# Optimization experiments

Measured on AMD Instinct MI355X. Metric: run time of the kernel, lower is better.

The kernel has to match this reference:

```python
import jax, jax.numpy as jnp
import numpy as np

DIM = 1024
HEADS = 16
DHEAD = 64
MAXLEN = 512
B = 8
N = 256   # sequence (x) length
M = 256   # memory (h) length; M + N <= MAXLEN
INNER = HEADS * DHEAD


def setup_inputs() -> dict:
    key = jax.random.key(0)
    ks = jax.random.split(key, 8)
    w = lambda k, shape: jax.random.normal(k, shape, jnp.float32) * 0.02
    return {
        "x": jax.random.normal(ks[0], (B, N, DIM), jnp.float32),
        "h": jax.random.normal(ks[1], (B, M, DIM), jnp.float32),
        "Wqkv": w(ks[2], (DIM, 3 * INNER)),
        "Wkr": w(ks[3], (DIM, INNER)),
        "R": jax.random.normal(ks[4], (2 * MAXLEN, DIM), jnp.float32),
        "u": jax.random.normal(ks[5], (DHEAD,), jnp.float32),
        "v": jax.random.normal(ks[6], (DHEAD,), jnp.float32),
        "Wout": w(ks[7], (INNER, DIM)),
        "max_len": MAXLEN,
    }


def reference(x, h, Wqkv, Wkr, R, u, v, Wout, max_len):
    b, n, dim = x.shape
    m = h.shape[1]
    t = m + n
    scale = DHEAD ** -0.5

    cat = jnp.concatenate([h, x], axis=1)                     # [b, t, dim]
    qkv = cat @ Wqkv                                          # [b, t, 3*inner]
    q, k, val = [s.reshape(b, t, HEADS, DHEAD).transpose(0, 2, 1, 3)
                 for s in jnp.split(qkv, 3, axis=-1)]          # [b, h, t, d]

    # shifts[i, j] = (j - i) mod 2L, sliced as in the torch buffer
    ar = jnp.arange(2 * max_len)
    shifts_full = (ar[None, :] - ar[:, None]) % (2 * max_len)
    shifts = shifts_full[:max_len, :max_len][m:m + n, :t]      # [n, t]

    kr = (R @ Wkr)[shifts]                                    # gather: [n, t, inner]
    kr = kr.reshape(n, t, HEADS, DHEAD).transpose(2, 0, 1, 3)  # [h, n, t, d]

    q = q[:, :, m:]                                           # [b, h, n, d]

    term_a = jnp.einsum('bhnd,bhmd->bhnm', q, k)
    term_b = jnp.einsum('bhnd,hnmd->bhnm', q, kr)
    term_c = jnp.einsum('d,bhmd->bhm', u, k)[:, :, None, :]    # broadcast over n
    term_d = jnp.einsum('d,hnmd->hnm', v, kr)[None]            # broadcast over b
    dots = (term_a + term_b + term_c + term_d) * scale         # [b, h, n, t]

    qi = jnp.arange(n)[:, None]
    jm = jnp.arange(m)[None, :]
    js = jnp.arange(n)[None, :]
    mem_mask = jnp.where(qi > jm, -jnp.inf, 0.0)               # [n, m]
    ar_mask = jnp.where(js > qi, -jnp.inf, 0.0)                # [n, n]
    bias = jnp.concatenate([mem_mask, ar_mask], axis=1)[None, None]  # [1,1,n,t]

    attn = jax.nn.softmax(dots + bias, axis=-1)
    out = jnp.einsum('bhnm,bhmd->bhnd', attn, val)             # [b, h, n, d]
    out = out.transpose(0, 2, 1, 3).reshape(b, n, INNER)
    return out @ Wout
```

## Files before the change

kernel.cpp:

```cpp
#include <hip/hip_runtime.h>
#include <hip/hip_bf16.h>
#include <math.h>

typedef unsigned short u16;
typedef short bf16x8 __attribute__((ext_vector_type(8)));
typedef float f32x4 __attribute__((ext_vector_type(4)));

__device__ __forceinline__ u16 f2b(float f) {
    __hip_bfloat16 h = __float2bfloat16(f);
    return *reinterpret_cast<u16*>(&h);
}
__device__ __forceinline__ float b2f(u16 v) {
    __hip_bfloat16 h;
    *reinterpret_cast<u16*>(&h) = v;
    return __bfloat162float(h);
}

__device__ __forceinline__ void gload_lds16(const void* g, void* l) {
    __builtin_amdgcn_global_load_lds(
        (const __attribute__((address_space(1))) void*)g,
        (__attribute__((address_space(3))) void*)l, 16, 0, 0);
}


struct EpiQKV4 {
    u16 *Q, *Kt, *Vt;
    __device__ void operator()(int rowp, int colp, f32x4 vals) const {
        int b = colp >> 9, pos = colp & 511;
        int sec = rowp >> 10, cc = rowp & 1023;
        int head = cc >> 6, d0 = cc & 63;
        if (sec == 0) {
            if (pos < 256) return;
            ushort4 o;
            o.x = f2b(vals[0] * 0.125f); o.y = f2b(vals[1] * 0.125f);
            o.z = f2b(vals[2] * 0.125f); o.w = f2b(vals[3] * 0.125f);
            *(ushort4*)(Q + (long)((head * 8 + b) * 256 + (pos - 256)) * 64 + d0) = o;
        } else if (sec == 1) {
            ushort4 o;
            o.x = f2b(vals[0]); o.y = f2b(vals[1]);
            o.z = f2b(vals[2]); o.w = f2b(vals[3]);
            *(ushort4*)(Kt + (long)((b * 16 + head) * 512 + pos) * 64 + d0) = o;
        } else {
            #pragma unroll
            for (int r = 0; r < 4; ++r)
                Vt[(long)((b * 16 + head) * 64 + d0 + r) * 512 + pos] = f2b(vals[r]);
        }
    }
};

struct EpiStoreBf {
    u16* C; long ldc; long strideZ;
    __device__ void operator()(int z, int row, int col, float val) const {
        C[(long)z * strideZ + (long)row * ldc + col] = f2b(val);
    }
};


template <typename Epi, bool AF32, bool ROWMAP>
__device__ __forceinline__ void gemm_bt_body(char* smem, int bx, int by, int bz,
                                             const void* __restrict__ Av, int lda, long strideAz,
                                             const u16* __restrict__ B, int ldb, long strideBz,
                                             int K, Epi epi) {
    constexpr int LDT = 56;
    u16* As = (u16*)smem;
    u16* Bs = As + 64 * LDT;
    int n0 = bx * 64, m0 = by * 64, z = bz;
    const u16* Bb = B + (long)z * strideBz + (long)n0 * ldb;
    int tid = threadIdx.x;
    int wave = tid >> 6, lane = tid & 63;
    int wm = wave >> 1, wn = wave & 1;
    int lrow = lane & 15, lquad = lane >> 4;
    int srow = tid >> 2, scol = (tid & 3) * 8;
    f32x4 acc[2][2] = {};
    for (int k0 = 0; k0 < K; k0 += 32) {
        if constexpr (AF32) {
            long arow = m0 + srow;
            if constexpr (ROWMAP) arow = (arow < 256) ? 768 + arow : 0;
            const float* src = (const float*)Av + (long)z * strideAz + arow * lda + k0 + scol;
            float4 f0 = *(const float4*)src;
            float4 f1 = *(const float4*)(src + 4);
            bf16x8 vv;
            vv[0] = (short)f2b(f0.x); vv[1] = (short)f2b(f0.y);
            vv[2] = (short)f2b(f0.z); vv[3] = (short)f2b(f0.w);
            vv[4] = (short)f2b(f1.x); vv[5] = (short)f2b(f1.y);
            vv[6] = (short)f2b(f1.z); vv[7] = (short)f2b(f1.w);
            *(bf16x8*)(As + srow * LDT + scol) = vv;
        } else {
            const u16* Ab = (const u16*)Av + (long)z * strideAz + (long)m0 * lda;
            *(bf16x8*)(As + srow * LDT + scol) = *(const bf16x8*)(Ab + (long)srow * lda + k0 + scol);
        }
        *(bf16x8*)(Bs + srow * LDT + scol) = *(const bf16x8*)(Bb + (long)srow * ldb + k0 + scol);
        __syncthreads();
        bf16x8 af[2], bfr[2];
        #pragma unroll
        for (int mt = 0; mt < 2; ++mt)
            af[mt] = *(const bf16x8*)(As + (wm * 32 + mt * 16 + lrow) * LDT + lquad * 8);
        #pragma unroll
        for (int nt = 0; nt < 2; ++nt)
            bfr[nt] = *(const bf16x8*)(Bs + (wn * 32 + nt * 16 + lrow) * LDT + lquad * 8);
        #pragma unroll
        for (int mt = 0; mt < 2; ++mt)
            #pragma unroll
            for (int nt = 0; nt < 2; ++nt)
                acc[mt][nt] = __builtin_amdgcn_mfma_f32_16x16x32_bf16(af[mt], bfr[nt], acc[mt][nt], 0, 0, 0);
        __syncthreads();
    }
    #pragma unroll
    for (int mt = 0; mt < 2; ++mt)
        #pragma unroll
        for (int nt = 0; nt < 2; ++nt)
            #pragma unroll
            for (int r = 0; r < 4; ++r) {
                int row = m0 + wm * 32 + mt * 16 + lquad * 4 + r;
                int col = n0 + wn * 32 + nt * 16 + lrow;
                epi(z, row, col, acc[mt][nt][r]);
            }
}

__global__ __launch_bounds__(256) void prep_kernel(const float* __restrict__ x,
                                                   const float* __restrict__ h,
                                                   u16* __restrict__ catBF,
                                                   const float* __restrict__ Wqkv, u16* __restrict__ WqkvT,
                                                   const float* __restrict__ Wkr,  u16* __restrict__ WkrT,
                                                   const float* __restrict__ Wout, u16* __restrict__ WoutT,
                                                   u16* __restrict__ vtGuard) {
    __shared__ float tile[32][33];
    int bid = blockIdx.x, tid = threadIdx.x;
    if (bid == 7168) {
        ((unsigned int*)vtGuard)[tid] = 0u;
        return;
    }
    if (bid < 2048) {
        int idx = (bid * 256 + tid) * 8;
        int c = idx & 1023, r = idx >> 10;
        int b = r >> 9, pos = r & 511;
        const float* src = (pos < 256) ? h + ((long)(b * 256 + pos) * 1024 + c)
                                       : x + ((long)(b * 256 + pos - 256) * 1024 + c);
        float4 f0 = *(const float4*)src;
        float4 f1 = *(const float4*)(src + 4);
        bf16x8 vv;
        vv[0] = (short)f2b(f0.x); vv[1] = (short)f2b(f0.y);
        vv[2] = (short)f2b(f0.z); vv[3] = (short)f2b(f0.w);
        vv[4] = (short)f2b(f1.x); vv[5] = (short)f2b(f1.y);
        vv[6] = (short)f2b(f1.z); vv[7] = (short)f2b(f1.w);
        *(bf16x8*)(catBF + idx) = vv;
        return;
    }
    const float* W; u16* WT; int nb, kb;
    if (bid < 5120) {
        int w = bid - 2048;
        W = Wqkv; WT = WqkvT;
        nb = (w % 96) * 32; kb = (w / 96) * 32;
        int tx = tid & 31, ty = tid >> 5;
        #pragma unroll
        for (int i = 0; i < 32; i += 8)
            tile[ty + i][tx] = W[(long)(kb + ty + i) * 3072 + nb + tx];
    } else {
        int w = bid - 5120;
        if (w < 1024) { W = Wkr; WT = WkrT; }
        else          { W = Wout; WT = WoutT; w -= 1024; }
        nb = (w & 31) * 32; kb = (w >> 5) * 32;
        int tx = tid & 31, ty = tid >> 5;
        #pragma unroll
        for (int i = 0; i < 32; i += 8)
            tile[ty + i][tx] = W[(long)(kb + ty + i) * 1024 + nb + tx];
    }
    __syncthreads();
    int row = tid >> 3;
    int c4 = (tid & 7) * 4;
    ushort4 o;
    o.x = f2b(tile[c4 + 0][row]);
    o.y = f2b(tile[c4 + 1][row]);
    o.z = f2b(tile[c4 + 2][row]);
    o.w = f2b(tile[c4 + 3][row]);
    *(ushort4*)(WT + (long)(nb + row) * 1024 + kb + c4) = o;
}

__global__ __launch_bounds__(256, 5) void qkv_rwg_kernel(const u16* __restrict__ A, const u16* __restrict__ B,
                                                         EpiQKV4 eq,
                                                         const float* __restrict__ R, const u16* __restrict__ WkrT,
                                                         u16* __restrict__ RWg) {
    __shared__ alignas(16) char smem[24576];
    int bid0 = blockIdx.x;
    if (bid0 < 80) {
        gemm_bt_body<EpiStoreBf, true, true>(smem, bid0 & 15, bid0 >> 4, 0,
            (const void*)R, 1024, 0L, WkrT, 1024, 0L, 1024, EpiStoreBf{RWg, 1024, 0});
        return;
    }
    int q = bid0 - 80;
    int xcd = q & 7, s = q >> 3;
    int G = xcd * 10 + (s >> 4);
    int w = s & 15;
    int m0, n0;
    if (G < 64) {
        int nchunk = G >> 4, mrow = G & 15;
        m0 = 1024 + mrow * 128 + (w & 1) * 64;
        n0 = (nchunk * 8 + (w >> 1)) * 128;
    } else {
        int G2 = G - 64;
        int nchunk = G2 >> 3, mrow = G2 & 7;
        m0 = mrow * 128 + (w & 1) * 64;
        int c = nchunk * 8 + (w >> 1);
        n0 = (c >> 1) * 512 + 256 + (c & 1) * 128;
    }
    int tid = threadIdx.x, wave = tid >> 6, lane = tid & 63;
    int lrow = lane & 15, lquad = lane >> 4;
    const u16* Ab = A + (long)m0 * 1024;
    const u16* Bb = B + (long)n0 * 1024;
    f32x4 acc[4][2] = {};

    auto stage = [&](int buf, int k0) {
        u16* Asb = (u16*)smem + buf * 6144;
        u16* Bsb = Asb + 2048;
        int row = tid >> 2, col = k0 + (tid & 3) * 8;
        gload_lds16(Ab + (long)row * 1024 + col, Asb + tid * 8);
        #pragma unroll
        for (int i = 0; i < 2; ++i)
            gload_lds16(Bb + (long)(i * 64 + row) * 1024 + col, Bsb + i * 2048 + tid * 8);
    };
    auto compute = [&](int buf) {
        u16* Asb = (u16*)smem + buf * 6144;
        u16* Bsb = Asb + 2048;
        bf16x8 af[4], bfr[2];
        #pragma unroll
        for (int mt = 0; mt < 4; ++mt)
            af[mt] = *(const bf16x8*)(Asb + (mt * 16 + lrow) * 32 + lquad * 8);
        #pragma unroll
        for (int nt = 0; nt < 2; ++nt)
            bfr[nt] = *(const bf16x8*)(Bsb + (wave * 32 + nt * 16 + lrow) * 32 + lquad * 8);
        #pragma unroll
        for (int mt = 0; mt < 4; ++mt)
            #pragma unroll
            for (int nt = 0; nt < 2; ++nt)
                acc[mt][nt] = __builtin_amdgcn_mfma_f32_16x16x32_bf16(af[mt], bfr[nt], acc[mt][nt], 0, 0, 0);
    };

    stage(0, 0);
    stage(1, 32);
    for (int t = 0; t < 31; ++t) {
        asm volatile("s_waitcnt vmcnt(3)" ::: "memory");
        __builtin_amdgcn_sched_barrier(0);
        __builtin_amdgcn_s_barrier();
        __builtin_amdgcn_sched_barrier(0);
        compute(t & 1);
        __builtin_amdgcn_sched_barrier(0);
        __builtin_amdgcn_s_barrier();
        __builtin_amdgcn_sched_barrier(0);
        if (t < 30) stage(t & 1, (t + 2) * 32);
    }
    asm volatile("s_waitcnt vmcnt(0)" ::: "memory");
    __builtin_amdgcn_sched_barrier(0);
    __builtin_amdgcn_s_barrier();
    __builtin_amdgcn_sched_barrier(0);
    compute(1);

    #pragma unroll
    for (int mt = 0; mt < 4; ++mt)
        #pragma unroll
        for (int nt = 0; nt < 2; ++nt) {
            int rowp = m0 + mt * 16 + lquad * 4;
            int colp = n0 + wave * 32 + nt * 16 + lrow;
            eq(rowp, colp, acc[mt][nt]);
        }
}

__global__ __launch_bounds__(256, 4) void outproj_kernel(const u16* __restrict__ A,
                                                         const u16* __restrict__ B,
                                                         float* __restrict__ out) {
    __shared__ alignas(16) char smem[16384];
    int bid = blockIdx.x;
    int n0 = (bid & 15) * 64, m0 = (bid >> 4) * 64;
    int tid = threadIdx.x, wave = tid >> 6, lane = tid & 63;
    int wm = wave >> 1, wn = wave & 1;
    int lrow = lane & 15, lquad = lane >> 4;
    const u16* Ab = A + (long)m0 * 1024;
    const u16* Bb = B + (long)n0 * 1024;
    f32x4 acc[2][2] = {};

    auto stage = [&](int buf, int k0) {
        u16* Asb = (u16*)smem + buf * 4096;
        u16* Bsb = Asb + 2048;
        int row = tid >> 2, col = k0 + (tid & 3) * 8;
        gload_lds16(Ab + (long)row * 1024 + col, Asb + tid * 8);
        gload_lds16(Bb + (long)row * 1024 + col, Bsb + tid * 8);
    };
    auto compute = [&](int buf) {
        u16* Asb = (u16*)smem + buf * 4096;
        u16* Bsb = Asb + 2048;
        bf16x8 af[2], bfr[2];
        #pragma unroll
        for (int mt = 0; mt < 2; ++mt)
            af[mt] = *(const bf16x8*)(Asb + (wm * 32 + mt * 16 + lrow) * 32 + lquad * 8);
        #pragma unroll
        for (int nt = 0; nt < 2; ++nt)
            bfr[nt] = *(const bf16x8*)(Bsb + (wn * 32 + nt * 16 + lrow) * 32 + lquad * 8);
        #pragma unroll
        for (int mt = 0; mt < 2; ++mt)
            #pragma unroll
            for (int nt = 0; nt < 2; ++nt)
                acc[mt][nt] = __builtin_amdgcn_mfma_f32_16x16x32_bf16(af[mt], bfr[nt], acc[mt][nt], 0, 0, 0);
    };

    stage(0, 0);
    stage(1, 32);
    for (int t = 0; t < 31; ++t) {
        asm volatile("s_waitcnt vmcnt(2)" ::: "memory");
        __builtin_amdgcn_sched_barrier(0);
        __builtin_amdgcn_s_barrier();
        __builtin_amdgcn_sched_barrier(0);
        compute(t & 1);
        __builtin_amdgcn_sched_barrier(0);
        __builtin_amdgcn_s_barrier();
        __builtin_amdgcn_sched_barrier(0);
        if (t < 30) stage(t & 1, (t + 2) * 32);
    }
    asm volatile("s_waitcnt vmcnt(0)" ::: "memory");
    __builtin_amdgcn_sched_barrier(0);
    __builtin_amdgcn_s_barrier();
    __builtin_amdgcn_sched_barrier(0);
    compute(1);

    #pragma unroll
    for (int mt = 0; mt < 2; ++mt)
        #pragma unroll
        for (int nt = 0; nt < 2; ++nt)
            #pragma unroll
            for (int r = 0; r < 4; ++r)
                out[(long)(m0 + wm * 32 + mt * 16 + lquad * 4 + r) * 1024
                    + n0 + wn * 32 + nt * 16 + lrow] = acc[mt][nt][r];
}

__global__ __launch_bounds__(256, 4) void attn_kernel(const u16* __restrict__ Qs,
                                                      const u16* __restrict__ Kt,
                                                      const u16* __restrict__ VT,
                                                      const u16* __restrict__ RWg,
                                                      const float* __restrict__ uvec,
                                                      const float* __restrict__ vvec,
                                                      u16* __restrict__ attnOut) {
    constexpr int LDSW = 328;
    __shared__ alignas(16) u16 SQ[32 * LDSW];
    __shared__ float red[2][4][32];
    int id = blockIdx.x;
    int bh = id & 127, it = id >> 7;
    int b = bh >> 4, h = bh & 15;
    int i0 = it * 32;
    int w0 = i0;
    int tid = threadIdx.x, wave = tid >> 6, lane = tid & 63;
    int lrow = lane & 15, lquad = lane >> 4;

    bf16x8 aq[2][2], aqv[2][2];
    #pragma unroll
    for (int iu = 0; iu < 2; ++iu) {
        const u16* qbase = Qs + (long)((h * 8 + b) * 256 + i0 + iu * 16 + lrow) * 64;
        bf16x8 q0 = *(const bf16x8*)(qbase + lquad * 8);
        bf16x8 q1 = *(const bf16x8*)(qbase + 32 + lquad * 8);
        #pragma unroll
        for (int j = 0; j < 8; ++j) {
            float f0 = b2f((u16)q0[j]), f1 = b2f((u16)q1[j]);
            aq[iu][0][j]  = (short)f2b(f0 + 0.125f * uvec[lquad * 8 + j]);
            aq[iu][1][j]  = (short)f2b(f1 + 0.125f * uvec[32 + lquad * 8 + j]);
            aqv[iu][0][j] = (short)f2b(f0 + 0.125f * vvec[lquad * 8 + j]);
            aqv[iu][1][j] = (short)f2b(f1 + 0.125f * vvec[32 + lquad * 8 + j]);
        }
    }

    const u16* rwbase = RWg + (long)(wave * 80) * 1024 + h * 64;
    #pragma unroll
    for (int t = 0; t < 5; ++t) {
        const u16* rp = rwbase + (long)(t * 16 + lrow) * 1024;
        bf16x8 br0 = *(const bf16x8*)(rp + lquad * 8);
        bf16x8 br1 = *(const bf16x8*)(rp + 32 + lquad * 8);
        int sc = wave * 80 + t * 16 + lrow;
        #pragma unroll
        for (int iu = 0; iu < 2; ++iu) {
            f32x4 qa = {0.f, 0.f, 0.f, 0.f};
            qa = __builtin_amdgcn_mfma_f32_16x16x32_bf16(aqv[iu][0], br0, qa, 0, 0, 0);
            qa = __builtin_amdgcn_mfma_f32_16x16x32_bf16(aqv[iu][1], br1, qa, 0, 0, 0);
            #pragma unroll
            for (int r = 0; r < 4; ++r)
                SQ[(iu * 16 + lquad * 4 + r) * LDSW + sc] = f2b(qa[r]);
        }
    }

    const u16* kbase = Kt + ((long)bh * 512 + w0 + wave * 80) * 64;
    bf16x8 bk0[5], bk1[5];
    #pragma unroll
    for (int t = 0; t < 5; ++t) {
        const u16* kp = kbase + (long)(t * 16 + lrow) * 64;
        bk0[t] = *(const bf16x8*)(kp + lquad * 8);
        bk1[t] = *(const bf16x8*)(kp + 32 + lquad * 8);
    }
    f32x4 acc[2][5];
    #pragma unroll
    for (int t = 0; t < 5; ++t)
        #pragma unroll
        for (int iu = 0; iu < 2; ++iu) {
            f32x4 a = {0.f, 0.f, 0.f, 0.f};
            a = __builtin_amdgcn_mfma_f32_16x16x32_bf16(aq[iu][0], bk0[t], a, 0, 0, 0);
            a = __builtin_amdgcn_mfma_f32_16x16x32_bf16(aq[iu][1], bk1[t], a, 0, 0, 0);
            acc[iu][t] = a;
        }
    __syncthreads();

    float m4[2][4];
    #pragma unroll
    for (int iu = 0; iu < 2; ++iu)
        #pragma unroll
        for (int r = 0; r < 4; ++r) m4[iu][r] = -1e30f;
    #pragma unroll
    for (int t = 0; t < 5; ++t) {
        int lj = wave * 80 + t * 16 + lrow;
        #pragma unroll
        for (int iu = 0; iu < 2; ++iu)
            #pragma unroll
            for (int r = 0; r < 4; ++r) {
                int rloc = iu * 16 + lquad * 4 + r;
                int d = lj - rloc;
                int dc = d < 0 ? 0 : (d > 256 ? 256 : d);
                bool ok = (unsigned)d <= 256u;
                float val = ok ? acc[iu][t][r] + b2f(SQ[rloc * LDSW + dc]) : -1e30f;
                acc[iu][t][r] = val;
                m4[iu][r] = fmaxf(m4[iu][r], val);
            }
    }
    #pragma unroll
    for (int iu = 0; iu < 2; ++iu)
        #pragma unroll
        for (int r = 0; r < 4; ++r) {
            #pragma unroll
            for (int off = 1; off < 16; off <<= 1)
                m4[iu][r] = fmaxf(m4[iu][r], __shfl_xor(m4[iu][r], off));
            if (lrow == 0) red[0][wave][iu * 16 + lquad * 4 + r] = m4[iu][r];
        }
    __syncthreads();

    float gmax[2][4];
    #pragma unroll
    for (int iu = 0; iu < 2; ++iu)
        #pragma unroll
        for (int r = 0; r < 4; ++r) {
            int row = iu * 16 + lquad * 4 + r;
            gmax[iu][r] = fmaxf(fmaxf(red[0][0][row], red[0][1][row]),
                                fmaxf(red[0][2][row], red[0][3][row]));
        }

    float s4[2][4] = {};
    #pragma unroll
    for (int t = 0; t < 5; ++t) {
        int lj = wave * 80 + t * 16 + lrow;
        #pragma unroll
        for (int iu = 0; iu < 2; ++iu)
            #pragma unroll
            for (int r = 0; r < 4; ++r) {
                float p = __expf(acc[iu][t][r] - gmax[iu][r]);
                s4[iu][r] += p;
                SQ[(iu * 16 + lquad * 4 + r) * LDSW + lj] = f2b(p);
            }
    }
    #pragma unroll
    for (int iu = 0; iu < 2; ++iu)
        #pragma unroll
        for (int r = 0; r < 4; ++r) {
            #pragma unroll
            for (int off = 1; off < 16; off <<= 1)
                s4[iu][r] += __shfl_xor(s4[iu][r], off);
            if (lrow == 0) red[1][wave][iu * 16 + lquad * 4 + r] = s4[iu][r];
        }
    __syncthreads();

    const u16* vbase = VT + ((long)bh * 64 + wave * 16 + lrow) * 512 + w0;
    f32x4 oacc[2] = {};
    bf16x8 vp[10];
    #pragma unroll
    for (int t = 0; t < 10; ++t)
        vp[t] = *(const bf16x8*)(vbase + t * 32 + lquad * 8);
    #pragma unroll
    for (int t = 0; t < 10; ++t)
        #pragma unroll
        for (int iu = 0; iu < 2; ++iu) {
            bf16x8 ap = *(const bf16x8*)(SQ + (iu * 16 + lrow) * LDSW + t * 32 + lquad * 8);
            oacc[iu] = __builtin_amdgcn_mfma_f32_16x16x32_bf16(ap, vp[t], oacc[iu], 0, 0, 0);
        }
    #pragma unroll
    for (int iu = 0; iu < 2; ++iu)
        #pragma unroll
        for (int r = 0; r < 4; ++r) {
            int row = iu * 16 + lquad * 4 + r;
            float inv = 1.0f / (red[1][0][row] + red[1][1][row] + red[1][2][row] + red[1][3][row]);
            attnOut[(long)(b * 256 + i0 + row) * 1024 + h * 64 + wave * 16 + lrow] = f2b(oacc[iu][r] * inv);
        }
}


extern "C" void kernel_launch(void* const* d_in, const int* in_sizes, int n_in,
                              void* d_out, int out_size, void* d_ws, size_t ws_size,
                              hipStream_t stream) {
    (void)in_sizes; (void)n_in; (void)out_size; (void)ws_size;
    const float* x    = (const float*)d_in[0];
    const float* h    = (const float*)d_in[1];
    const float* Wqkv = (const float*)d_in[2];
    const float* Wkr  = (const float*)d_in[3];
    const float* R    = (const float*)d_in[4];
    const float* u    = (const float*)d_in[5];
    const float* v    = (const float*)d_in[6];
    const float* Wout = (const float*)d_in[7];
    float* out = (float*)d_out;

    char* ws = (char*)d_ws;
    size_t off = 0;
    auto alloc = [&](size_t bytes) -> void* {
        void* p = ws + off;
        off = (off + bytes + 255) & ~(size_t)255;
        return p;
    };
    u16* catBF  = (u16*)alloc(4096L * 1024 * 2);
    u16* WqkvT  = (u16*)alloc(3072L * 1024 * 2);
    u16* WkrT   = (u16*)alloc(1024L * 1024 * 2);
    u16* WoutT  = (u16*)alloc(1024L * 1024 * 2);
    u16* RWg    = (u16*)alloc(320L * 1024 * 2);
    u16* Q      = (u16*)alloc(16L * 8 * 256 * 64 * 2);
    u16* Kt     = (u16*)alloc(8L * 16 * 512 * 64 * 2);
    u16* VT     = (u16*)alloc(8L * 16 * 64 * 512 * 2 + 1024);
    u16* attnO  = (u16*)alloc(2048L * 1024 * 2);
    u16* vtGuard = VT + 8L * 16 * 64 * 512;

    prep_kernel<<<7169, 256, 0, stream>>>(x, h, catBF, Wqkv, WqkvT, Wkr, WkrT, Wout, WoutT, vtGuard);
    qkv_rwg_kernel<<<1360, 256, 0, stream>>>(WqkvT, catBF, EpiQKV4{Q, Kt, VT}, R, WkrT, RWg);
    attn_kernel<<<1024, 256, 0, stream>>>(Q, Kt, VT, RWg, u, v, attnO);
    outproj_kernel<<<512, 256, 0, stream>>>(attnO, WoutT, out);
}
```

Measured before the change: 168.8 us.

## Enlarge QKV GEMM tiles to 128x128, swizzle LDS, set MFMA priority in attention

The QKV GEMM block tile grows from 64x128 to 128x128, with a 2x2 wave layout and 4x4 MFMA accumulators per wave. This halves the grid and raises operand reuse per LDS load. An XOR-like column permutation is applied when staging global-to-LDS in both the QKV and out-projection GEMMs, with matching reads, to reduce LDS bank conflicts. The RWg blocks move to the end of the grid, and s_setprio is raised around the MFMA loops in the attention kernel. The trade-off is fewer blocks and more registers and LDS per block, hence launch bounds of 4 instead of 5, which lowers occupancy.

```diff
diff --git a/kernel.cpp b/kernel.cpp
--- a/kernel.cpp
+++ b/kernel.cpp
@@ -176,69 +176,75 @@
     *(ushort4*)(WT + (long)(nb + row) * 1024 + kb + c4) = o;
 }
 
-__global__ __launch_bounds__(256, 5) void qkv_rwg_kernel(const u16* __restrict__ A, const u16* __restrict__ B,
+__global__ __launch_bounds__(256, 4) void qkv_rwg_kernel(const u16* __restrict__ A, const u16* __restrict__ B,
                                                          EpiQKV4 eq,
                                                          const float* __restrict__ R, const u16* __restrict__ WkrT,
                                                          u16* __restrict__ RWg) {
-    __shared__ alignas(16) char smem[24576];
+    __shared__ alignas(16) char smem[32768];
     int bid0 = blockIdx.x;
-    if (bid0 < 80) {
-        gemm_bt_body<EpiStoreBf, true, true>(smem, bid0 & 15, bid0 >> 4, 0,
+    if (bid0 >= 640) {
+        int bid2 = bid0 - 640;
+        gemm_bt_body<EpiStoreBf, true, true>(smem, bid2 & 15, bid2 >> 4, 0,
             (const void*)R, 1024, 0L, WkrT, 1024, 0L, 1024, EpiStoreBf{RWg, 1024, 0});
         return;
     }
-    int q = bid0 - 80;
-    int xcd = q & 7, s = q >> 3;
-    int G = xcd * 10 + (s >> 4);
-    int w = s & 15;
+    int xcd = bid0 & 7, s = bid0 >> 3;
+    int G = xcd * 10 + (s >> 3);
+    int w = s & 7;
     int m0, n0;
     if (G < 64) {
         int nchunk = G >> 4, mrow = G & 15;
-        m0 = 1024 + mrow * 128 + (w & 1) * 64;
-        n0 = (nchunk * 8 + (w >> 1)) * 128;
+        m0 = 1024 + mrow * 128;
+        n0 = (nchunk * 8 + w) * 128;
     } else {
         int G2 = G - 64;
         int nchunk = G2 >> 3, mrow = G2 & 7;
-        m0 = mrow * 128 + (w & 1) * 64;
-        int c = nchunk * 8 + (w >> 1);
+        m0 = mrow * 128;
+        int c = nchunk * 8 + w;
         n0 = (c >> 1) * 512 + 256 + (c & 1) * 128;
     }
     int tid = threadIdx.x, wave = tid >> 6, lane = tid & 63;
+    int wm = wave >> 1, wn = wave & 1;
     int lrow = lane & 15, lquad = lane >> 4;
     const u16* Ab = A + (long)m0 * 1024;
     const u16* Bb = B + (long)n0 * 1024;
-    f32x4 acc[4][2] = {};
+    f32x4 acc[4][4] = {};
+
+    int scperm = (((tid & 3) - ((tid >> 3) & 3)) & 3) * 8;
+    int rsl = ((lquad + (lrow >> 1)) & 3) * 8;
 
     auto stage = [&](int buf, int k0) {
-        u16* Asb = (u16*)smem + buf * 6144;
-        u16* Bsb = Asb + 2048;
-        int row = tid >> 2, col = k0 + (tid & 3) * 8;
-        gload_lds16(Ab + (long)row * 1024 + col, Asb + tid * 8);
-        #pragma unroll
-        for (int i = 0; i < 2; ++i)
-            gload_lds16(Bb + (long)(i * 64 + row) * 1024 + col, Bsb + i * 2048 + tid * 8);
+        u16* Asb = (u16*)smem + buf * 8192;
+        u16* Bsb = Asb + 4096;
+        int col = k0 + scperm;
+        #pragma unroll
+        for (int i = 0; i < 2; ++i) {
+            int rowb = i * 64 + (tid >> 2);
+            gload_lds16(Ab + (long)rowb * 1024 + col, Asb + i * 2048 + tid * 8);
+            gload_lds16(Bb + (long)rowb * 1024 + col, Bsb + i * 2048 + tid * 8);
+        }
     };
     auto compute = [&](int buf) {
-        u16* Asb = (u16*)smem + buf * 6144;
-        u16* Bsb = Asb + 2048;
-        bf16x8 af[4], bfr[2];
+        u16* Asb = (u16*)smem + buf * 8192;
+        u16* Bsb = Asb + 4096;
+        bf16x8 af[4], bfr[4];
         #pragma unroll
         for (int mt = 0; mt < 4; ++mt)
-            af[mt] = *(const bf16x8*)(Asb + (mt * 16 + lrow) * 32 + lquad * 8);
-        #pragma unroll
-        for (int nt = 0; nt < 2; ++nt)
-            bfr[nt] = *(const bf16x8*)(Bsb + (wave * 32 + nt * 16 + lrow) * 32 + lquad * 8);
+            af[mt] = *(const bf16x8*)(Asb + (wm * 64 + mt * 16 + lrow) * 32 + rsl);
+        #pragma unroll
+        for (int nt = 0; nt < 4; ++nt)
+            bfr[nt] = *(const bf16x8*)(Bsb + (wn * 64 + nt * 16 + lrow) * 32 + rsl);
         #pragma unroll
         for (int mt = 0; mt < 4; ++mt)
             #pragma unroll
-            for (int nt = 0; nt < 2; ++nt)
+            for (int nt = 0; nt < 4; ++nt)
                 acc[mt][nt] = __builtin_amdgcn_mfma_f32_16x16x32_bf16(af[mt], bfr[nt], acc[mt][nt], 0, 0, 0);
     };
 
     stage(0, 0);
     stage(1, 32);
     for (int t = 0; t < 31; ++t) {
-        asm volatile("s_waitcnt vmcnt(3)" ::: "memory");
+        asm volatile("s_waitcnt vmcnt(4)" ::: "memory");
         __builtin_amdgcn_sched_barrier(0);
         __builtin_amdgcn_s_barrier();
         __builtin_amdgcn_sched_barrier(0);
@@ -257,9 +263,9 @@
     #pragma unroll
     for (int mt = 0; mt < 4; ++mt)
         #pragma unroll
-        for (int nt = 0; nt < 2; ++nt) {
-            int rowp = m0 + mt * 16 + lquad * 4;
-            int colp = n0 + wave * 32 + nt * 16 + lrow;
+        for (int nt = 0; nt < 4; ++nt) {
+            int rowp = m0 + wm * 64 + mt * 16 + lquad * 4;
+            int colp = n0 + wn * 64 + nt * 16 + lrow;
             eq(rowp, colp, acc[mt][nt]);
         }
 }
@@ -277,10 +283,13 @@
     const u16* Bb = B + (long)n0 * 1024;
     f32x4 acc[2][2] = {};
 
+    int scperm = (((tid & 3) - ((tid >> 3) & 3)) & 3) * 8;
+    int rsl = ((lquad + (lrow >> 1)) & 3) * 8;
+
     auto stage = [&](int buf, int k0) {
         u16* Asb = (u16*)smem + buf * 4096;
         u16* Bsb = Asb + 2048;
-        int row = tid >> 2, col = k0 + (tid & 3) * 8;
+        int row = tid >> 2, col = k0 + scperm;
         gload_lds16(Ab + (long)row * 1024 + col, Asb + tid * 8);
         gload_lds16(Bb + (long)row * 1024 + col, Bsb + tid * 8);
     };
@@ -290,10 +299,10 @@
         bf16x8 af[2], bfr[2];
         #pragma unroll
         for (int mt = 0; mt < 2; ++mt)
-            af[mt] = *(const bf16x8*)(Asb + (wm * 32 + mt * 16 + lrow) * 32 + lquad * 8);
+            af[mt] = *(const bf16x8*)(Asb + (wm * 32 + mt * 16 + lrow) * 32 + rsl);
         #pragma unroll
         for (int nt = 0; nt < 2; ++nt)
-            bfr[nt] = *(const bf16x8*)(Bsb + (wn * 32 + nt * 16 + lrow) * 32 + lquad * 8);
+            bfr[nt] = *(const bf16x8*)(Bsb + (wn * 32 + nt * 16 + lrow) * 32 + rsl);
         #pragma unroll
         for (int mt = 0; mt < 2; ++mt)
             #pragma unroll
@@ -391,6 +400,7 @@
         bk1[t] = *(const bf16x8*)(kp + 32 + lquad * 8);
     }
     f32x4 acc[2][5];
+    __builtin_amdgcn_s_setprio(1);
     #pragma unroll
     for (int t = 0; t < 5; ++t)
         #pragma unroll
@@ -400,6 +410,7 @@
             a = __builtin_amdgcn_mfma_f32_16x16x32_bf16(aq[iu][1], bk1[t], a, 0, 0, 0);
             acc[iu][t] = a;
         }
+    __builtin_amdgcn_s_setprio(0);
     __syncthreads();
 
     float m4[2][4];
@@ -474,6 +485,7 @@
     #pragma unroll
     for (int t = 0; t < 10; ++t)
         vp[t] = *(const bf16x8*)(vbase + t * 32 + lquad * 8);
+    __builtin_amdgcn_s_setprio(1);
     #pragma unroll
     for (int t = 0; t < 10; ++t)
         #pragma unroll
@@ -481,6 +493,7 @@
             bf16x8 ap = *(const bf16x8*)(SQ + (iu * 16 + lrow) * LDSW + t * 32 + lquad * 8);
             oacc[iu] = __builtin_amdgcn_mfma_f32_16x16x32_bf16(ap, vp[t], oacc[iu], 0, 0, 0);
         }
+    __builtin_amdgcn_s_setprio(0);
     #pragma unroll
     for (int iu = 0; iu < 2; ++iu)
         #pragma unroll
@@ -525,7 +538,7 @@
     u16* vtGuard = VT + 8L * 16 * 64 * 512;
 
     prep_kernel<<<7169, 256, 0, stream>>>(x, h, catBF, Wqkv, WqkvT, Wkr, WkrT, Wout, WoutT, vtGuard);
-    qkv_rwg_kernel<<<1360, 256, 0, stream>>>(WqkvT, catBF, EpiQKV4{Q, Kt, VT}, R, WkrT, RWg);
+    qkv_rwg_kernel<<<720, 256, 0, stream>>>(WqkvT, catBF, EpiQKV4{Q, Kt, VT}, R, WkrT, RWg);
     attn_kernel<<<1024, 256, 0, stream>>>(Q, Kt, VT, RWg, u, v, attnO);
     outproj_kernel<<<512, 256, 0, stream>>>(attnO, WoutT, out);
 }
```

Result: faster. 159.8 us (-5.3%).
